# Kernel tuning notes

Hardware: AMD Instinct MI355X
Metric: run time of the kernel (lower is better)

## Reference

```python
import jax, jax.numpy as jnp
import numpy as np

TOP_K = 2  # num_experts_per_tok


def setup_inputs() -> dict:
    key = jax.random.key(0)
    ks = jax.random.split(key, 5)
    B, S, D, M, E = 4, 2048, 2048, 2048, 8
    x = jax.random.normal(ks[0], (B, S, D), dtype=jnp.float32)
    gate_kernel = jax.random.normal(ks[1], (D, E), dtype=jnp.float32) / np.sqrt(D)
    wi_0 = jax.random.normal(ks[2], (E, D, M), dtype=jnp.float32) / np.sqrt(D)
    wi_1 = jax.random.normal(ks[3], (E, D, M), dtype=jnp.float32) / np.sqrt(D)
    wo = jax.random.normal(ks[4], (E, M, D), dtype=jnp.float32) / np.sqrt(M)
    return {"x": x, "gate_kernel": gate_kernel, "wi_0": wi_0, "wi_1": wi_1, "wo": wo}


def reference(x, gate_kernel, wi_0, wi_1, wo):
    E = gate_kernel.shape[-1]
    # Gate logits: (B, S, E)
    gate_logits = jnp.einsum("bsd,de->bse", x, gate_kernel)
    # Top-k routing, then softmax over the selected experts' logits
    top_k_weights, top_k_indices = jax.lax.top_k(gate_logits, TOP_K)
    top_k_weights = jax.nn.softmax(top_k_weights.astype(jnp.float32), axis=-1).astype(x.dtype)
    # Dense combine weights per expert: (B, S, E)
    combine_w = jnp.sum(
        jax.nn.one_hot(top_k_indices, E, dtype=x.dtype) * top_k_weights[..., None], axis=-2
    )
    # Grouped GEMM (dense-masked form, as in MaxText dense_matmul path)
    h0 = jnp.einsum("bsd,edm->bsem", x, wi_0)  # (B, S, E, M)
    h1 = jnp.einsum("bsd,edm->bsem", x, wi_1)
    h = jax.nn.silu(h0) * h1 * combine_w[..., None]
    out = jnp.einsum("bsem,emd->bsd", h, wo)  # (B, S, D)
    return out
```

## Files before the change

kernel.cpp:

```cpp
#include <hip/hip_runtime.h>
#include <hip/hip_bf16.h>
#include <stdint.h>

#define TT   8192
#define DD   2048
#define MM   2048
#define NE   8

typedef float f32x4 __attribute__((ext_vector_type(4)));
typedef short s16x8 __attribute__((ext_vector_type(8)));
typedef unsigned int u32;
typedef unsigned long long u64;

static __device__ __forceinline__ short f2bf(float f) {
  __hip_bfloat16 h = __float2bfloat16(f);
  short s;
  __builtin_memcpy(&s, &h, 2);
  return s;
}

static __device__ __forceinline__ void gload_lds16(const short* g, short* lds) {
  __builtin_amdgcn_global_load_lds(
      (const __attribute__((address_space(1))) u32*)g,
      (__attribute__((address_space(3))) u32*)lds, 16, 0, 0);
}

__global__ __launch_bounds__(256) void tcvt_kernel(
    const float* __restrict__ w0, const float* __restrict__ w1, const float* __restrict__ w2,
    short* __restrict__ o0, short* __restrict__ o1, short* __restrict__ o2) {
  __shared__ short tile[64][65];
  const int bz = blockIdx.z;
  const float* in; short* out;
  if (bz < 8)       { in = w0; out = o0; }
  else if (bz < 16) { in = w1; out = o1; }
  else              { in = w2; out = o2; }
  const int ex = bz & 7;
  const float* src = in + (size_t)ex * DD * MM;
  short* dst = out + (size_t)ex * DD * MM;
  const int r0 = blockIdx.y * 64;
  const int c0 = blockIdx.x * 64;
  const int t = threadIdx.x;
  const int rr = t >> 4, cc = (t & 15) * 4;
  #pragma unroll
  for (int i = 0; i < 4; i++) {
    int row = rr + i * 16;
    f32x4 v = *(const f32x4*)(src + (size_t)(r0 + row) * MM + c0 + cc);
    tile[cc + 0][row] = f2bf(v[0]);
    tile[cc + 1][row] = f2bf(v[1]);
    tile[cc + 2][row] = f2bf(v[2]);
    tile[cc + 3][row] = f2bf(v[3]);
  }
  __syncthreads();
  const int orow = t >> 2, c8 = (t & 3) * 16;
  s16x8 v0, v1;
  #pragma unroll
  for (int i = 0; i < 8; i++) { v0[i] = tile[orow][c8 + i]; v1[i] = tile[orow][c8 + 8 + i]; }
  short* dp = dst + (size_t)(c0 + orow) * DD + r0 + c8;
  *(s16x8*)(dp) = v0;
  *(s16x8*)(dp + 8) = v1;
}

__global__ __launch_bounds__(256) void gate_kernel(const float* __restrict__ x,
    const float* __restrict__ gk, int* __restrict__ counts,
    int* __restrict__ tkidx, float* __restrict__ tkw, short* __restrict__ xbf) {
  int t = blockIdx.x;
  const float* xr = x + (size_t)t * DD;
  const int d0 = threadIdx.x * 8;
  f32x4 a = *(const f32x4*)(xr + d0);
  f32x4 b = *(const f32x4*)(xr + d0 + 4);
  s16x8 v;
  v[0]=f2bf(a[0]); v[1]=f2bf(a[1]); v[2]=f2bf(a[2]); v[3]=f2bf(a[3]);
  v[4]=f2bf(b[0]); v[5]=f2bf(b[1]); v[6]=f2bf(b[2]); v[7]=f2bf(b[3]);
  *(s16x8*)(xbf + (size_t)t * DD + d0) = v;

  float acc[NE];
  #pragma unroll
  for (int e = 0; e < NE; e++) acc[e] = 0.f;
  #pragma unroll
  for (int j = 0; j < 8; j++) {
    float xv = (j < 4) ? a[j] : b[j - 4];
    const float* g = gk + (size_t)(d0 + j) * NE;
    #pragma unroll
    for (int e = 0; e < NE; e++) acc[e] += xv * g[e];
  }
  #pragma unroll
  for (int e = 0; e < NE; e++) {
    #pragma unroll
    for (int off = 32; off >= 1; off >>= 1)
      acc[e] += __shfl_xor(acc[e], off, 64);
  }
  __shared__ float red[4][NE];
  int wid = threadIdx.x >> 6;
  int lane = threadIdx.x & 63;
  if (lane == 0) {
    #pragma unroll
    for (int e = 0; e < NE; e++) red[wid][e] = acc[e];
  }
  __syncthreads();
  if (threadIdx.x == 0) {
    float l[NE];
    #pragma unroll
    for (int e = 0; e < NE; e++) l[e] = red[0][e] + red[1][e] + red[2][e] + red[3][e];
    int i1 = 0; float v1 = l[0];
    #pragma unroll
    for (int e = 1; e < NE; e++) if (l[e] > v1) { v1 = l[e]; i1 = e; }
    int i2 = -1; float v2 = -1e30f;
    #pragma unroll
    for (int e = 0; e < NE; e++) if (e != i1 && l[e] > v2) { v2 = l[e]; i2 = e; }
    float p = __expf(v2 - v1);
    float inv = 1.f / (1.f + p);
    tkidx[t*2]   = i1; tkidx[t*2+1] = i2;
    tkw[t*2]     = inv; tkw[t*2+1]  = p * inv;
    atomicAdd(&counts[i1], 1);
    atomicAdd(&counts[i2], 1);
  }
}

__global__ __launch_bounds__(256) void scatter_kernel(const int* __restrict__ counts,
    int* __restrict__ offsets, const int* __restrict__ tkidx,
    const float* __restrict__ tkw, int* __restrict__ ltok, float* __restrict__ lwt,
    int* __restrict__ slots) {
  const int e = blockIdx.x;
  const int tid = threadIdx.x;
  const int wid = tid >> 6, lane = tid & 63;
  __shared__ int base_s;
  __shared__ int wsum[4];
  if (tid == 0) {
    int s = 0;
    #pragma unroll
    for (int i = 0; i < NE; i++) {
      if (e == 0) offsets[i] = s;
      if (i < e) s += counts[i];
      else if (e == 0) s += counts[i];
    }
    if (e == 0) offsets[NE] = s;
    int bs = 0;
    for (int i = 0; i < e; i++) bs += counts[i];
    base_s = bs;
  }
  __syncthreads();
  int base = base_s;
  for (int it = 0; it < (TT * 2) / 256; it++) {
    int i = it * 256 + tid;
    bool m = (tkidx[i] == e);
    u64 b = __ballot(m);
    if (lane == 0) wsum[wid] = __popcll(b);
    __syncthreads();
    int pre = 0;
    #pragma unroll
    for (int w = 0; w < 4; w++) if (w < wid) pre += wsum[w];
    int tot = wsum[0] + wsum[1] + wsum[2] + wsum[3];
    int rank = __popcll(b & ((lane == 0) ? 0ull : ((1ull << lane) - 1ull)));
    if (m) {
      int dst = base + pre + rank;
      ltok[dst] = i >> 1;
      lwt[dst]  = tkw[i];
      slots[i]  = dst;
    }
    __syncthreads();
    base += tot;
  }
}

__global__ __launch_bounds__(256) void combine_kernel(const float* __restrict__ comb,
    const int* __restrict__ slots, float* __restrict__ out) {
  const int t = blockIdx.x;
  const int s0 = slots[2 * t], s1 = slots[2 * t + 1];
  const f32x4* p0 = (const f32x4*)(comb + (size_t)s0 * DD);
  const f32x4* p1 = (const f32x4*)(comb + (size_t)s1 * DD);
  f32x4* po = (f32x4*)(out + (size_t)t * DD);
  #pragma unroll
  for (int i = 0; i < 2; i++) {
    int idx = threadIdx.x + i * 256;
    po[idx] = p0[idx] + p1[idx];
  }
}

__device__ __forceinline__ void find_seg(const int* __restrict__ offsets, int tile, int bm,
                                         int& e, int& row0, int& rows, int& seg) {
  e = -1; row0 = 0; rows = 0; seg = 0;
  int accT = 0, prev = offsets[0];
  #pragma unroll
  for (int i = 0; i < NE; i++) {
    int nxt = offsets[i+1];
    int cnt = nxt - prev;
    int nt = (cnt + bm - 1) / bm;
    if (e < 0 && tile < accT + nt) { e = i; row0 = (tile - accT) * bm; rows = cnt; seg = prev; }
    accT += nt; prev = nxt;
  }
}

__device__ __forceinline__ void xcd_map(int ypx, int& tile, int& nyi) {
  const int bid = blockIdx.y * gridDim.x + blockIdx.x;
  const int xcd = bid & 7;
  const int i = bid >> 3;
  tile = i / ypx;
  nyi  = xcd * ypx + (i % ypx);
}

#define MAXT1 136

__global__ __launch_bounds__(256, 2) void gemm1_fast(
    const short* __restrict__ xbf,
    const short* __restrict__ w0t, const short* __restrict__ w1t,
    const int* __restrict__ offsets,
    const int* __restrict__ ltok, const float* __restrict__ lwt,
    short* __restrict__ hbuf) {
  __shared__ short As[128 * 64];
  __shared__ short B0s[128 * 64];
  __shared__ short B1s[128 * 64];
  __shared__ float w_s[128];

  int tile, nyi;
  xcd_map(2, tile, nyi);
  const int n0 = nyi * 128;
  int e, row0, rows, seg;
  find_seg(offsets, tile, 128, e, row0, rows, seg);
  if (e < 0) return;

  const int tid = threadIdx.x;
  const int lane = tid & 63, wid = tid >> 6;
  if (tid < 128) {
    int gr = row0 + tid;
    w_s[tid] = (gr < rows) ? lwt[seg + gr] : 0.f;
  }

  const int swz = ((lane & 7) ^ (lane >> 3)) * 8;
  const short* abase[4];
  const short* b0base[4];
  const short* b1base[4];
  #pragma unroll
  for (int c = 0; c < 4; c++) {
    int chunk = wid * 4 + c;
    int r = chunk * 8 + (lane >> 3);
    int gr = row0 + r; if (gr >= rows) gr = rows - 1;
    int tok = ltok[seg + gr];
    abase[c]  = xbf + (size_t)tok * DD + swz;
    int n = n0 + r;
    b0base[c] = w0t + ((size_t)e * MM + n) * DD + swz;
    b1base[c] = w1t + ((size_t)e * MM + n) * DD + swz;
  }

  const int wr = wid >> 1, wc = wid & 1;
  const int lr = lane & 15;
  const int kq = (lane >> 4) * 8;

  f32x4 acc0[4][4], acc1[4][4];
  #pragma unroll
  for (int i = 0; i < 4; i++)
    #pragma unroll
    for (int j = 0; j < 4; j++) { acc0[i][j] = 0.f; acc1[i][j] = 0.f; }

  for (int k0 = 0; k0 < DD; k0 += 64) {
    #pragma unroll
    for (int c = 0; c < 4; c++) {
      int chunk = wid * 4 + c;
      gload_lds16(abase[c]  + k0, As  + chunk * 512);
      gload_lds16(b0base[c] + k0, B0s + chunk * 512);
      gload_lds16(b1base[c] + k0, B1s + chunk * 512);
    }
    __syncthreads();

    #pragma unroll
    for (int ks = 0; ks < 2; ks++) {
      s16x8 a[4], b0[4], b1[4];
      #pragma unroll
      for (int mi = 0; mi < 4; mi++) {
        int row = wr * 64 + mi * 16 + lr;
        int koff = (ks * 32 + kq) ^ ((row & 7) * 8);
        a[mi] = *(const s16x8*)&As[row * 64 + koff];
      }
      #pragma unroll
      for (int ni = 0; ni < 4; ni++) {
        int row = wc * 64 + ni * 16 + lr;
        int koff = (ks * 32 + kq) ^ ((row & 7) * 8);
        b0[ni] = *(const s16x8*)&B0s[row * 64 + koff];
        b1[ni] = *(const s16x8*)&B1s[row * 64 + koff];
      }
      #pragma unroll
      for (int mi = 0; mi < 4; mi++)
        #pragma unroll
        for (int ni = 0; ni < 4; ni++) {
          acc0[mi][ni] = __builtin_amdgcn_mfma_f32_16x16x32_bf16(a[mi], b0[ni], acc0[mi][ni], 0, 0, 0);
          acc1[mi][ni] = __builtin_amdgcn_mfma_f32_16x16x32_bf16(a[mi], b1[ni], acc1[mi][ni], 0, 0, 0);
        }
    }
    __syncthreads();
  }

  const int lq = lane >> 4;
  #pragma unroll
  for (int mi = 0; mi < 4; mi++) {
    #pragma unroll
    for (int jj = 0; jj < 4; jj++) {
      int r = wr * 64 + mi * 16 + lq * 4 + jj;
      int gr = row0 + r;
      if (gr < rows) {
        float wgt = w_s[r];
        size_t hrow = (size_t)(seg + gr) * MM + n0;
        #pragma unroll
        for (int ni = 0; ni < 4; ni++) {
          int c = wc * 64 + ni * 16 + lr;
          float g = acc0[mi][ni][jj];
          float u = acc1[mi][ni][jj];
          float act = g / (1.f + __expf(-g));
          hbuf[hrow + c] = f2bf(act * u * wgt);
        }
      }
    }
  }
}

#define MAXT2 264

__global__ __launch_bounds__(256, 2) void gemm2_fast(
    const short* __restrict__ hbuf,
    const short* __restrict__ wot,
    const int* __restrict__ offsets,
    float* __restrict__ comb) {
  __shared__ short As[64 * 64];
  __shared__ short B0s[128 * 64];
  __shared__ short B1s[128 * 64];

  int tile, nyi;
  xcd_map(1, tile, nyi);
  const int n0 = nyi * 256;
  int e, row0, rows, seg;
  find_seg(offsets, tile, 64, e, row0, rows, seg);
  if (e < 0) return;

  const int tid = threadIdx.x;
  const int lane = tid & 63, wid = tid >> 6;

  const int swz = ((lane & 7) ^ (lane >> 3)) * 8;
  const short* abase[2];
  #pragma unroll
  for (int c = 0; c < 2; c++) {
    int chunk = wid * 2 + c;
    int r = chunk * 8 + (lane >> 3);
    int gr = row0 + r; if (gr >= rows) gr = rows - 1;
    abase[c] = hbuf + (size_t)(seg + gr) * MM + swz;
  }
  const short* b0base[4];
  const short* b1base[4];
  #pragma unroll
  for (int c = 0; c < 4; c++) {
    int chunk = wid * 4 + c;
    int r = chunk * 8 + (lane >> 3);
    b0base[c] = wot + ((size_t)e * DD + n0 + r) * MM + swz;
    b1base[c] = wot + ((size_t)e * DD + n0 + 128 + r) * MM + swz;
  }

  const int wr = wid >> 1, wc = wid & 1;
  const int lr = lane & 15;
  const int kq = (lane >> 4) * 8;

  f32x4 acc0[2][4], acc1[2][4];
  #pragma unroll
  for (int i = 0; i < 2; i++)
    #pragma unroll
    for (int j = 0; j < 4; j++) { acc0[i][j] = 0.f; acc1[i][j] = 0.f; }

  for (int k0 = 0; k0 < MM; k0 += 64) {
    #pragma unroll
    for (int c = 0; c < 2; c++) {
      int chunk = wid * 2 + c;
      gload_lds16(abase[c] + k0, As + chunk * 512);
    }
    #pragma unroll
    for (int c = 0; c < 4; c++) {
      int chunk = wid * 4 + c;
      gload_lds16(b0base[c] + k0, B0s + chunk * 512);
      gload_lds16(b1base[c] + k0, B1s + chunk * 512);
    }
    __syncthreads();

    #pragma unroll
    for (int ks = 0; ks < 2; ks++) {
      s16x8 a[2], b0[4], b1[4];
      #pragma unroll
      for (int mi = 0; mi < 2; mi++) {
        int row = wr * 32 + mi * 16 + lr;
        int koff = (ks * 32 + kq) ^ ((row & 7) * 8);
        a[mi] = *(const s16x8*)&As[row * 64 + koff];
      }
      #pragma unroll
      for (int ni = 0; ni < 4; ni++) {
        int row = wc * 64 + ni * 16 + lr;
        int koff = (ks * 32 + kq) ^ ((row & 7) * 8);
        b0[ni] = *(const s16x8*)&B0s[row * 64 + koff];
        b1[ni] = *(const s16x8*)&B1s[row * 64 + koff];
      }
      #pragma unroll
      for (int mi = 0; mi < 2; mi++)
        #pragma unroll
        for (int ni = 0; ni < 4; ni++) {
          acc0[mi][ni] = __builtin_amdgcn_mfma_f32_16x16x32_bf16(a[mi], b0[ni], acc0[mi][ni], 0, 0, 0);
          acc1[mi][ni] = __builtin_amdgcn_mfma_f32_16x16x32_bf16(a[mi], b1[ni], acc1[mi][ni], 0, 0, 0);
        }
    }
    __syncthreads();
  }

  const int lq = lane >> 4;
  #pragma unroll
  for (int mi = 0; mi < 2; mi++) {
    #pragma unroll
    for (int jj = 0; jj < 4; jj++) {
      int r = wr * 32 + mi * 16 + lq * 4 + jj;
      int gr = row0 + r;
      if (gr < rows) {
        size_t orow = (size_t)(seg + gr) * DD + n0;
        #pragma unroll
        for (int ni = 0; ni < 4; ni++) {
          int c = wc * 64 + ni * 16 + lr;
          comb[orow + c] = acc0[mi][ni][jj];
          comb[orow + 128 + c] = acc1[mi][ni][jj];
        }
      }
    }
  }
}

extern "C" void kernel_launch(void* const* d_in, const int* in_sizes, int n_in,
                              void* d_out, int out_size, void* d_ws, size_t ws_size,
                              hipStream_t stream) {
  const float* x   = (const float*)d_in[0];
  const float* gk  = (const float*)d_in[1];
  const float* wi0 = (const float*)d_in[2];
  const float* wi1 = (const float*)d_in[3];
  const float* wo  = (const float*)d_in[4];
  float* out = (float*)d_out;

  char* w = (char*)d_ws;
  int*   counts  = (int*)(w);
  int*   offsets = (int*)(w + 256);
  int*   tkidx   = (int*)(w + 1024);
  float* tkw     = (float*)(w + 1024 + 65536);
  int*   ltok    = (int*)(w + 1024 + 2*65536);
  float* lwt     = (float*)(w + 1024 + 3*65536);
  int*   slots   = (int*)(w + 1024 + 4*65536);
  short* xbf  = (short*)(w + 524288);
  short* hbuf = xbf + (size_t)TT * DD;
  short* w0t  = hbuf + (size_t)2 * TT * MM;
  short* w1t  = w0t + (size_t)NE * DD * MM;
  short* wot  = w1t + (size_t)NE * DD * MM;
  float* comb = (float*)w0t;

  hipMemsetAsync(counts, 0, 64, stream);

  gate_kernel<<<TT, 256, 0, stream>>>(x, gk, counts, tkidx, tkw, xbf);
  scatter_kernel<<<NE, 256, 0, stream>>>(counts, offsets, tkidx, tkw, ltok, lwt, slots);
  tcvt_kernel<<<dim3(MM/64, DD/64, 24), 256, 0, stream>>>(wi0, wi1, wo, w0t, w1t, wot);

  gemm1_fast<<<dim3(MAXT1, MM/128), 256, 0, stream>>>(xbf, w0t, w1t, offsets, ltok, lwt, hbuf);
  gemm2_fast<<<dim3(MAXT2, DD/256), 256, 0, stream>>>(hbuf, wot, offsets, comb);
  combine_kernel<<<TT, 256, 0, stream>>>(comb, slots, out);
}
```

Measured before the change: 904.8 us.

## Rewrite gemm2 with 256x256 tiles, double-buffered LDS pipeline, and bf16 combine buffer

The down-projection GEMM now uses 512-thread blocks with 256x256 output tiles. Its LDS is double-buffered, and global-to-LDS prefetch is interleaved with MFMA phases using explicit vmcnt waits, barriers and setprio. This raises data reuse per tile and hides load latency. The intermediate per-slot outputs are also stored as bf16 instead of fp32, which halves combine traffic at some precision cost. The larger tiles waste more work on partially filled expert segments, and the hand-written waitcnt scheduling risks races.

Measured after the change: 890.7 us. No clear change (-1.6%).

```diff
diff --git a/kernel.cpp b/kernel.cpp
--- a/kernel.cpp
+++ b/kernel.cpp
@@ -18,12 +18,23 @@
   __builtin_memcpy(&s, &h, 2);
   return s;
 }
+static __device__ __forceinline__ float bf2f(short s) {
+  u32 u = ((u32)(unsigned short)s) << 16;
+  float f;
+  __builtin_memcpy(&f, &u, 4);
+  return f;
+}
 
 static __device__ __forceinline__ void gload_lds16(const short* g, short* lds) {
   __builtin_amdgcn_global_load_lds(
       (const __attribute__((address_space(1))) u32*)g,
       (__attribute__((address_space(3))) u32*)lds, 16, 0, 0);
 }
+
+#define VM2()  asm volatile("s_waitcnt vmcnt(2)" ::: "memory")
+#define VM0()  asm volatile("s_waitcnt vmcnt(0)" ::: "memory")
+#define LG0()  asm volatile("s_waitcnt lgkmcnt(0)" ::: "memory")
+#define BAR()  __builtin_amdgcn_s_barrier()
 
 __global__ __launch_bounds__(256) void tcvt_kernel(
     const float* __restrict__ w0, const float* __restrict__ w1, const float* __restrict__ w2,
@@ -162,18 +173,22 @@
   }
 }
 
-__global__ __launch_bounds__(256) void combine_kernel(const float* __restrict__ comb,
+__global__ __launch_bounds__(256) void combine_kernel(const short* __restrict__ comb,
     const int* __restrict__ slots, float* __restrict__ out) {
   const int t = blockIdx.x;
   const int s0 = slots[2 * t], s1 = slots[2 * t + 1];
-  const f32x4* p0 = (const f32x4*)(comb + (size_t)s0 * DD);
-  const f32x4* p1 = (const f32x4*)(comb + (size_t)s1 * DD);
-  f32x4* po = (f32x4*)(out + (size_t)t * DD);
-  #pragma unroll
-  for (int i = 0; i < 2; i++) {
-    int idx = threadIdx.x + i * 256;
-    po[idx] = p0[idx] + p1[idx];
-  }
+  const int idx = threadIdx.x;
+  s16x8 a = *(const s16x8*)(comb + (size_t)s0 * DD + idx * 8);
+  s16x8 b = *(const s16x8*)(comb + (size_t)s1 * DD + idx * 8);
+  f32x4 o0, o1;
+  #pragma unroll
+  for (int j = 0; j < 4; j++) {
+    o0[j] = bf2f(a[j]) + bf2f(b[j]);
+    o1[j] = bf2f(a[4 + j]) + bf2f(b[4 + j]);
+  }
+  float* po = out + (size_t)t * DD + idx * 8;
+  *(f32x4*)(po) = o0;
+  *(f32x4*)(po + 4) = o1;
 }
 
 __device__ __forceinline__ void find_seg(const int* __restrict__ offsets, int tile, int bm,
@@ -311,111 +326,231 @@
   }
 }
 
-#define MAXT2 264
-
-__global__ __launch_bounds__(256, 2) void gemm2_fast(
+#define MAXT2 72
+
+__global__ __launch_bounds__(512, 2) void gemm2_fast(
     const short* __restrict__ hbuf,
     const short* __restrict__ wot,
     const int* __restrict__ offsets,
-    float* __restrict__ comb) {
-  __shared__ short As[64 * 64];
-  __shared__ short B0s[128 * 64];
-  __shared__ short B1s[128 * 64];
+    short* __restrict__ comb) {
+  __shared__ short As[2][256 * 64];
+  __shared__ short Bs[2][256 * 64];
 
   int tile, nyi;
   xcd_map(1, tile, nyi);
   const int n0 = nyi * 256;
   int e, row0, rows, seg;
-  find_seg(offsets, tile, 64, e, row0, rows, seg);
+  find_seg(offsets, tile, 256, e, row0, rows, seg);
   if (e < 0) return;
 
   const int tid = threadIdx.x;
   const int lane = tid & 63, wid = tid >> 6;
-
-  const int swz = ((lane & 7) ^ (lane >> 3)) * 8;
-  const short* abase[2];
-  #pragma unroll
-  for (int c = 0; c < 2; c++) {
-    int chunk = wid * 2 + c;
-    int r = chunk * 8 + (lane >> 3);
-    int gr = row0 + r; if (gr >= rows) gr = rows - 1;
-    abase[c] = hbuf + (size_t)(seg + gr) * MM + swz;
-  }
-  const short* b0base[4];
-  const short* b1base[4];
-  #pragma unroll
-  for (int c = 0; c < 4; c++) {
-    int chunk = wid * 4 + c;
-    int r = chunk * 8 + (lane >> 3);
-    b0base[c] = wot + ((size_t)e * DD + n0 + r) * MM + swz;
-    b1base[c] = wot + ((size_t)e * DD + n0 + 128 + r) * MM + swz;
-  }
-
-  const int wr = wid >> 1, wc = wid & 1;
+  const int srow = tid >> 3;
+  const int swz = ((tid & 7) ^ (srow & 7)) * 8;
+
+  const short* aP[2][2];
+  const short* bP[2][2];
+  #pragma unroll
+  for (int h = 0; h < 2; h++)
+    #pragma unroll
+    for (int rd = 0; rd < 2; rd++) {
+      int gr = row0 + h * 128 + rd * 64 + srow;
+      if (gr >= rows) gr = rows - 1;
+      aP[h][rd] = hbuf + (size_t)(seg + gr) * MM + swz;
+      int n = n0 + h * 128 + rd * 64 + srow;
+      bP[h][rd] = wot + ((size_t)e * DD + n) * MM + swz;
+    }
+  const short* aP00 = aP[0][0]; const short* aP01 = aP[0][1];
+  const short* aP10 = aP[1][0]; const short* aP11 = aP[1][1];
+  const short* bP00 = bP[0][0]; const short* bP01 = bP[0][1];
+  const short* bP10 = bP[1][0]; const short* bP11 = bP[1][1];
+
+  const int wr = wid >> 2, wn = wid & 3;
   const int lr = lane & 15;
   const int kq = (lane >> 4) * 8;
-
-  f32x4 acc0[2][4], acc1[2][4];
-  #pragma unroll
-  for (int i = 0; i < 2; i++)
-    #pragma unroll
-    for (int j = 0; j < 4; j++) { acc0[i][j] = 0.f; acc1[i][j] = 0.f; }
-
-  for (int k0 = 0; k0 < MM; k0 += 64) {
-    #pragma unroll
-    for (int c = 0; c < 2; c++) {
-      int chunk = wid * 2 + c;
-      gload_lds16(abase[c] + k0, As + chunk * 512);
-    }
-    #pragma unroll
-    for (int c = 0; c < 4; c++) {
-      int chunk = wid * 4 + c;
-      gload_lds16(b0base[c] + k0, B0s + chunk * 512);
-      gload_lds16(b1base[c] + k0, B1s + chunk * 512);
-    }
-    __syncthreads();
-
-    #pragma unroll
-    for (int ks = 0; ks < 2; ks++) {
-      s16x8 a[2], b0[4], b1[4];
-      #pragma unroll
-      for (int mi = 0; mi < 2; mi++) {
-        int row = wr * 32 + mi * 16 + lr;
-        int koff = (ks * 32 + kq) ^ ((row & 7) * 8);
-        a[mi] = *(const s16x8*)&As[row * 64 + koff];
-      }
-      #pragma unroll
-      for (int ni = 0; ni < 4; ni++) {
-        int row = wc * 64 + ni * 16 + lr;
-        int koff = (ks * 32 + kq) ^ ((row & 7) * 8);
-        b0[ni] = *(const s16x8*)&B0s[row * 64 + koff];
-        b1[ni] = *(const s16x8*)&B1s[row * 64 + koff];
-      }
-      #pragma unroll
-      for (int mi = 0; mi < 2; mi++)
-        #pragma unroll
-        for (int ni = 0; ni < 4; ni++) {
-          acc0[mi][ni] = __builtin_amdgcn_mfma_f32_16x16x32_bf16(a[mi], b0[ni], acc0[mi][ni], 0, 0, 0);
-          acc1[mi][ni] = __builtin_amdgcn_mfma_f32_16x16x32_bf16(a[mi], b1[ni], acc1[mi][ni], 0, 0, 0);
-        }
-    }
-    __syncthreads();
-  }
-
   const int lq = lane >> 4;
-  #pragma unroll
-  for (int mi = 0; mi < 2; mi++) {
+
+  f32x4 acc[8][4];
+  #pragma unroll
+  for (int i = 0; i < 8; i++)
+    #pragma unroll
+    for (int j = 0; j < 4; j++) acc[i][j] = 0.f;
+
+  int brow_[4], bkey_[4];
+  #pragma unroll
+  for (int ni = 0; ni < 4; ni++) {
+    brow_[ni] = wn * 64 + ni * 16 + lr;
+    bkey_[ni] = (brow_[ni] & 7) * 8;
+  }
+  int arowL_[4], akeyL_[4], arowH_[4], akeyH_[4];
+  #pragma unroll
+  for (int mi = 0; mi < 4; mi++) {
+    arowL_[mi] = wr * 128 + mi * 16 + lr;        akeyL_[mi] = (arowL_[mi] & 7) * 8;
+    arowH_[mi] = wr * 128 + (mi + 4) * 16 + lr;  akeyH_[mi] = (arowH_[mi] & 7) * 8;
+  }
+
+  const int wofs = wid * 512;
+  auto stA0 = [&](int buf, int kof) {
+    short* d = &As[buf][0];
+    gload_lds16(aP00 + kof, d + wofs);
+    gload_lds16(aP01 + kof, d + 4096 + wofs);
+  };
+  auto stA1 = [&](int buf, int kof) {
+    short* d = &As[buf][128 * 64];
+    gload_lds16(aP10 + kof, d + wofs);
+    gload_lds16(aP11 + kof, d + 4096 + wofs);
+  };
+  auto stB0 = [&](int buf, int kof) {
+    short* d = &Bs[buf][0];
+    gload_lds16(bP00 + kof, d + wofs);
+    gload_lds16(bP01 + kof, d + 4096 + wofs);
+  };
+  auto stB1 = [&](int buf, int kof) {
+    short* d = &Bs[buf][128 * 64];
+    gload_lds16(bP10 + kof, d + wofs);
+    gload_lds16(bP11 + kof, d + 4096 + wofs);
+  };
+
+  stA0(0, 0); stB0(0, 0); stB1(0, 0); stA1(0, 0);
+  stA0(1, 64);
+  VM2();
+  BAR();
+
+  const int NIT = (MM / 64) / 2;
+  s16x8 av[4], bv[4], bw[4];
+
+  for (int it = 0; it < NIT; ++it) {
+    const bool pf = (it + 1 < NIT);
+    const int kb  = (2 * it + 1) * 64;
+    const int kna = (2 * it + 2) * 64;
+    const int knb = (2 * it + 3) * 64;
+
+    #pragma unroll
+    for (int mi = 0; mi < 4; mi++) av[mi] = *(const s16x8*)&As[0][arowL_[mi] * 64 + (kq ^ akeyL_[mi])];
+    #pragma unroll
+    for (int ni = 0; ni < 4; ni++) bv[ni] = *(const s16x8*)&Bs[0][brow_[ni] * 64 + (kq ^ bkey_[ni])];
+    stB0(1, kb);
+    BAR(); LG0();
+    __builtin_amdgcn_s_setprio(1);
+    #pragma unroll
+    for (int mi = 0; mi < 4; mi++)
+      #pragma unroll
+      for (int ni = 0; ni < 4; ni++)
+        acc[mi][ni] = __builtin_amdgcn_mfma_f32_16x16x32_bf16(av[mi], bv[ni], acc[mi][ni], 0, 0, 0);
+    __builtin_amdgcn_s_setprio(0);
+    BAR();
+
+    #pragma unroll
+    for (int mi = 0; mi < 4; mi++) av[mi] = *(const s16x8*)&As[0][arowH_[mi] * 64 + (kq ^ akeyH_[mi])];
+    stB1(1, kb);
+    BAR(); LG0();
+    __builtin_amdgcn_s_setprio(1);
+    #pragma unroll
+    for (int mi = 0; mi < 4; mi++)
+      #pragma unroll
+      for (int ni = 0; ni < 4; ni++)
+        acc[mi + 4][ni] = __builtin_amdgcn_mfma_f32_16x16x32_bf16(av[mi], bv[ni], acc[mi + 4][ni], 0, 0, 0);
+    __builtin_amdgcn_s_setprio(0);
+    BAR();
+
+    #pragma unroll
+    for (int mi = 0; mi < 4; mi++) av[mi] = *(const s16x8*)&As[0][arowL_[mi] * 64 + ((32 + kq) ^ akeyL_[mi])];
+    #pragma unroll
+    for (int ni = 0; ni < 4; ni++) bw[ni] = *(const s16x8*)&Bs[0][brow_[ni] * 64 + ((32 + kq) ^ bkey_[ni])];
+    stA1(1, kb);
+    BAR(); LG0();
+    __builtin_amdgcn_s_setprio(1);
+    #pragma unroll
+    for (int mi = 0; mi < 4; mi++)
+      #pragma unroll
+      for (int ni = 0; ni < 4; ni++)
+        acc[mi][ni] = __builtin_amdgcn_mfma_f32_16x16x32_bf16(av[mi], bw[ni], acc[mi][ni], 0, 0, 0);
+    __builtin_amdgcn_s_setprio(0);
+    BAR();
+
+    #pragma unroll
+    for (int mi = 0; mi < 4; mi++) av[mi] = *(const s16x8*)&As[0][arowH_[mi] * 64 + ((32 + kq) ^ akeyH_[mi])];
+    if (pf) stA0(0, kna);
+    BAR(); LG0();
+    __builtin_amdgcn_s_setprio(1);
+    #pragma unroll
+    for (int mi = 0; mi < 4; mi++)
+      #pragma unroll
+      for (int ni = 0; ni < 4; ni++)
+        acc[mi + 4][ni] = __builtin_amdgcn_mfma_f32_16x16x32_bf16(av[mi], bw[ni], acc[mi + 4][ni], 0, 0, 0);
+    __builtin_amdgcn_s_setprio(0);
+    if (pf) { VM2(); } else { VM0(); }
+    BAR();
+
+    #pragma unroll
+    for (int mi = 0; mi < 4; mi++) av[mi] = *(const s16x8*)&As[1][arowL_[mi] * 64 + (kq ^ akeyL_[mi])];
+    #pragma unroll
+    for (int ni = 0; ni < 4; ni++) bv[ni] = *(const s16x8*)&Bs[1][brow_[ni] * 64 + (kq ^ bkey_[ni])];
+    if (pf) stB0(0, kna);
+    BAR(); LG0();
+    __builtin_amdgcn_s_setprio(1);
+    #pragma unroll
+    for (int mi = 0; mi < 4; mi++)
+      #pragma unroll
+      for (int ni = 0; ni < 4; ni++)
+        acc[mi][ni] = __builtin_amdgcn_mfma_f32_16x16x32_bf16(av[mi], bv[ni], acc[mi][ni], 0, 0, 0);
+    __builtin_amdgcn_s_setprio(0);
+    BAR();
+
+    #pragma unroll
+    for (int mi = 0; mi < 4; mi++) av[mi] = *(const s16x8*)&As[1][arowH_[mi] * 64 + (kq ^ akeyH_[mi])];
+    if (pf) stB1(0, kna);
+    BAR(); LG0();
+    __builtin_amdgcn_s_setprio(1);
+    #pragma unroll
+    for (int mi = 0; mi < 4; mi++)
+      #pragma unroll
+      for (int ni = 0; ni < 4; ni++)
+        acc[mi + 4][ni] = __builtin_amdgcn_mfma_f32_16x16x32_bf16(av[mi], bv[ni], acc[mi + 4][ni], 0, 0, 0);
+    __builtin_amdgcn_s_setprio(0);
+    BAR();
+
+    #pragma unroll
+    for (int mi = 0; mi < 4; mi++) av[mi] = *(const s16x8*)&As[1][arowL_[mi] * 64 + ((32 + kq) ^ akeyL_[mi])];
+    #pragma unroll
+    for (int ni = 0; ni < 4; ni++) bw[ni] = *(const s16x8*)&Bs[1][brow_[ni] * 64 + ((32 + kq) ^ bkey_[ni])];
+    if (pf) stA1(0, kna);
+    BAR(); LG0();
+    __builtin_amdgcn_s_setprio(1);
+    #pragma unroll
+    for (int mi = 0; mi < 4; mi++)
+      #pragma unroll
+      for (int ni = 0; ni < 4; ni++)
+        acc[mi][ni] = __builtin_amdgcn_mfma_f32_16x16x32_bf16(av[mi], bw[ni], acc[mi][ni], 0, 0, 0);
+    __builtin_amdgcn_s_setprio(0);
+    BAR();
+
+    #pragma unroll
+    for (int mi = 0; mi < 4; mi++) av[mi] = *(const s16x8*)&As[1][arowH_[mi] * 64 + ((32 + kq) ^ akeyH_[mi])];
+    if (pf) stA0(1, knb);
+    BAR(); LG0();
+    __builtin_amdgcn_s_setprio(1);
+    #pragma unroll
+    for (int mi = 0; mi < 4; mi++)
+      #pragma unroll
+      for (int ni = 0; ni < 4; ni++)
+        acc[mi + 4][ni] = __builtin_amdgcn_mfma_f32_16x16x32_bf16(av[mi], bw[ni], acc[mi + 4][ni], 0, 0, 0);
+    __builtin_amdgcn_s_setprio(0);
+    if (pf) { VM2(); BAR(); }
+  }
+
+  #pragma unroll
+  for (int mi = 0; mi < 8; mi++) {
     #pragma unroll
     for (int jj = 0; jj < 4; jj++) {
-      int r = wr * 32 + mi * 16 + lq * 4 + jj;
+      int r = wr * 128 + mi * 16 + lq * 4 + jj;
       int gr = row0 + r;
       if (gr < rows) {
         size_t orow = (size_t)(seg + gr) * DD + n0;
         #pragma unroll
         for (int ni = 0; ni < 4; ni++) {
-          int c = wc * 64 + ni * 16 + lr;
-          comb[orow + c] = acc0[mi][ni][jj];
-          comb[orow + 128 + c] = acc1[mi][ni][jj];
+          int c = wn * 64 + ni * 16 + lr;
+          comb[orow + c] = f2bf(acc[mi][ni][jj]);
         }
       }
     }
@@ -445,7 +580,7 @@
   short* w0t  = hbuf + (size_t)2 * TT * MM;
   short* w1t  = w0t + (size_t)NE * DD * MM;
   short* wot  = w1t + (size_t)NE * DD * MM;
-  float* comb = (float*)w0t;
+  short* comb = w0t;
 
   hipMemsetAsync(counts, 0, 64, stream);
 
@@ -454,6 +589,6 @@
   tcvt_kernel<<<dim3(MM/64, DD/64, 24), 256, 0, stream>>>(wi0, wi1, wo, w0t, w1t, wot);
 
   gemm1_fast<<<dim3(MAXT1, MM/128), 256, 0, stream>>>(xbf, w0t, w1t, offsets, ltok, lwt, hbuf);
-  gemm2_fast<<<dim3(MAXT2, DD/256), 256, 0, stream>>>(hbuf, wot, offsets, comb);
+  gemm2_fast<<<dim3(MAXT2, DD/256), 512, 0, stream>>>(hbuf, wot, offsets, comb);
   combine_kernel<<<TT, 256, 0, stream>>>(comb, slots, out);
 }
```

## Fuse weight conversion into gate and gemm1, enlarge gemm2 tile, bf16 combine buffer

Applied to the files above, without the earlier changes.

Folds the wi0/wi1 bf16 transpose-convert blocks into the gate kernel launch and the wo conversion into the gemm1 launch as extra blocks, so conversion overlaps other work and one launch goes away. gemm2 moves from 64-row to 128-row M tiles, doubling accumulators per wave. The per-slot combine buffer is stored in bf16 instead of fp32, halving its write and read traffic. This costs extra output rounding, higher register pressure in gemm2, and wo-conversion blocks now contend with gemm1 compute.

Result: faster. 839.2 us, median of 2 (-7.3%).

```diff
diff --git a/kernel.cpp b/kernel.cpp
--- a/kernel.cpp
+++ b/kernel.cpp
@@ -18,6 +18,12 @@
   __builtin_memcpy(&s, &h, 2);
   return s;
 }
+static __device__ __forceinline__ float bf2f(short s) {
+  u32 u = ((u32)(unsigned short)s) << 16;
+  float f;
+  __builtin_memcpy(&f, &u, 4);
+  return f;
+}
 
 static __device__ __forceinline__ void gload_lds16(const short* g, short* lds) {
   __builtin_amdgcn_global_load_lds(
@@ -25,45 +31,52 @@
       (__attribute__((address_space(3))) u32*)lds, 16, 0, 0);
 }
 
-__global__ __launch_bounds__(256) void tcvt_kernel(
-    const float* __restrict__ w0, const float* __restrict__ w1, const float* __restrict__ w2,
-    short* __restrict__ o0, short* __restrict__ o1, short* __restrict__ o2) {
+#define GCVT01  (16 * 32 * 32)
+
+__global__ __launch_bounds__(256) void gate_fused(
+    const float* __restrict__ x, const float* __restrict__ gk,
+    int* __restrict__ counts, int* __restrict__ tkidx, float* __restrict__ tkw,
+    short* __restrict__ xbf,
+    const float* __restrict__ wi0, const float* __restrict__ wi1,
+    short* __restrict__ o0, short* __restrict__ o1) {
   __shared__ short tile[64][65];
-  const int bz = blockIdx.z;
-  const float* in; short* out;
-  if (bz < 8)       { in = w0; out = o0; }
-  else if (bz < 16) { in = w1; out = o1; }
-  else              { in = w2; out = o2; }
-  const int ex = bz & 7;
-  const float* src = in + (size_t)ex * DD * MM;
-  short* dst = out + (size_t)ex * DD * MM;
-  const int r0 = blockIdx.y * 64;
-  const int c0 = blockIdx.x * 64;
-  const int t = threadIdx.x;
-  const int rr = t >> 4, cc = (t & 15) * 4;
-  #pragma unroll
-  for (int i = 0; i < 4; i++) {
-    int row = rr + i * 16;
-    f32x4 v = *(const f32x4*)(src + (size_t)(r0 + row) * MM + c0 + cc);
-    tile[cc + 0][row] = f2bf(v[0]);
-    tile[cc + 1][row] = f2bf(v[1]);
-    tile[cc + 2][row] = f2bf(v[2]);
-    tile[cc + 3][row] = f2bf(v[3]);
-  }
-  __syncthreads();
-  const int orow = t >> 2, c8 = (t & 3) * 16;
-  s16x8 v0, v1;
-  #pragma unroll
-  for (int i = 0; i < 8; i++) { v0[i] = tile[orow][c8 + i]; v1[i] = tile[orow][c8 + 8 + i]; }
-  short* dp = dst + (size_t)(c0 + orow) * DD + r0 + c8;
-  *(s16x8*)(dp) = v0;
-  *(s16x8*)(dp + 8) = v1;
-}
-
-__global__ __launch_bounds__(256) void gate_kernel(const float* __restrict__ x,
-    const float* __restrict__ gk, int* __restrict__ counts,
-    int* __restrict__ tkidx, float* __restrict__ tkw, short* __restrict__ xbf) {
-  int t = blockIdx.x;
+  __shared__ float red[4][NE];
+
+  const int bid = blockIdx.x;
+  if (bid >= TT) {
+    const int idx = bid - TT;
+    const int wz = idx >> 10;
+    const float* in  = (wz < 8) ? wi0 : wi1;
+    short* out       = (wz < 8) ? o0 : o1;
+    const int ex = wz & 7;
+    const int rem = idx & 1023;
+    const int r0 = (rem >> 5) * 64;
+    const int c0 = (rem & 31) * 64;
+    const float* src = in + (size_t)ex * DD * MM;
+    short* dst = out + (size_t)ex * DD * MM;
+    const int t = threadIdx.x;
+    const int rr = t >> 4, cc = (t & 15) * 4;
+    #pragma unroll
+    for (int i = 0; i < 4; i++) {
+      int row = rr + i * 16;
+      f32x4 v = *(const f32x4*)(src + (size_t)(r0 + row) * MM + c0 + cc);
+      tile[cc + 0][row] = f2bf(v[0]);
+      tile[cc + 1][row] = f2bf(v[1]);
+      tile[cc + 2][row] = f2bf(v[2]);
+      tile[cc + 3][row] = f2bf(v[3]);
+    }
+    __syncthreads();
+    const int orow = t >> 2, c8 = (t & 3) * 16;
+    s16x8 v0, v1;
+    #pragma unroll
+    for (int i = 0; i < 8; i++) { v0[i] = tile[orow][c8 + i]; v1[i] = tile[orow][c8 + 8 + i]; }
+    short* dp = dst + (size_t)(c0 + orow) * DD + r0 + c8;
+    *(s16x8*)(dp) = v0;
+    *(s16x8*)(dp + 8) = v1;
+    return;
+  }
+
+  const int t = bid;
   const float* xr = x + (size_t)t * DD;
   const int d0 = threadIdx.x * 8;
   f32x4 a = *(const f32x4*)(xr + d0);
@@ -89,7 +102,6 @@
     for (int off = 32; off >= 1; off >>= 1)
       acc[e] += __shfl_xor(acc[e], off, 64);
   }
-  __shared__ float red[4][NE];
   int wid = threadIdx.x >> 6;
   int lane = threadIdx.x & 63;
   if (lane == 0) {
@@ -162,18 +174,22 @@
   }
 }
 
-__global__ __launch_bounds__(256) void combine_kernel(const float* __restrict__ comb,
+__global__ __launch_bounds__(256) void combine_kernel(const short* __restrict__ comb,
     const int* __restrict__ slots, float* __restrict__ out) {
   const int t = blockIdx.x;
   const int s0 = slots[2 * t], s1 = slots[2 * t + 1];
-  const f32x4* p0 = (const f32x4*)(comb + (size_t)s0 * DD);
-  const f32x4* p1 = (const f32x4*)(comb + (size_t)s1 * DD);
-  f32x4* po = (f32x4*)(out + (size_t)t * DD);
-  #pragma unroll
-  for (int i = 0; i < 2; i++) {
-    int idx = threadIdx.x + i * 256;
-    po[idx] = p0[idx] + p1[idx];
-  }
+  const int idx = threadIdx.x;
+  s16x8 a = *(const s16x8*)(comb + (size_t)s0 * DD + idx * 8);
+  s16x8 b = *(const s16x8*)(comb + (size_t)s1 * DD + idx * 8);
+  f32x4 o0, o1;
+  #pragma unroll
+  for (int j = 0; j < 4; j++) {
+    o0[j] = bf2f(a[j]) + bf2f(b[j]);
+    o1[j] = bf2f(a[4 + j]) + bf2f(b[4 + j]);
+  }
+  float* po = out + (size_t)t * DD + idx * 8;
+  *(f32x4*)(po) = o0;
+  *(f32x4*)(po + 4) = o1;
 }
 
 __device__ __forceinline__ void find_seg(const int* __restrict__ offsets, int tile, int bm,
@@ -198,21 +214,58 @@
   nyi  = xcd * ypx + (i % ypx);
 }
 
-#define MAXT1 136
-
-__global__ __launch_bounds__(256, 2) void gemm1_fast(
+#define G1TILES 136
+#define G1GRID  (G1TILES * 16)
+#define GOGRID  (8 * 32 * 32)
+
+__global__ __launch_bounds__(256, 2) void gemm1_fused(
     const short* __restrict__ xbf,
     const short* __restrict__ w0t, const short* __restrict__ w1t,
     const int* __restrict__ offsets,
     const int* __restrict__ ltok, const float* __restrict__ lwt,
-    short* __restrict__ hbuf) {
+    short* __restrict__ hbuf,
+    const float* __restrict__ wo, short* __restrict__ wot) {
   __shared__ short As[128 * 64];
   __shared__ short B0s[128 * 64];
   __shared__ short B1s[128 * 64];
   __shared__ float w_s[128];
 
-  int tile, nyi;
-  xcd_map(2, tile, nyi);
+  const int bid = blockIdx.x;
+  if (bid >= G1GRID) {
+    short (*tile)[65] = (short(*)[65])As;
+    const int idx = bid - G1GRID;
+    const int ex = idx >> 10;
+    const int rem = idx & 1023;
+    const int r0 = (rem >> 5) * 64;
+    const int c0 = (rem & 31) * 64;
+    const float* src = wo + (size_t)ex * DD * MM;
+    short* dst = wot + (size_t)ex * DD * MM;
+    const int t = threadIdx.x;
+    const int rr = t >> 4, cc = (t & 15) * 4;
+    #pragma unroll
+    for (int i = 0; i < 4; i++) {
+      int row = rr + i * 16;
+      f32x4 v = *(const f32x4*)(src + (size_t)(r0 + row) * MM + c0 + cc);
+      tile[cc + 0][row] = f2bf(v[0]);
+      tile[cc + 1][row] = f2bf(v[1]);
+      tile[cc + 2][row] = f2bf(v[2]);
+      tile[cc + 3][row] = f2bf(v[3]);
+    }
+    __syncthreads();
+    const int orow = t >> 2, c8 = (t & 3) * 16;
+    s16x8 v0, v1;
+    #pragma unroll
+    for (int i = 0; i < 8; i++) { v0[i] = tile[orow][c8 + i]; v1[i] = tile[orow][c8 + 8 + i]; }
+    short* dp = dst + (size_t)(c0 + orow) * DD + r0 + c8;
+    *(s16x8*)(dp) = v0;
+    *(s16x8*)(dp + 8) = v1;
+    return;
+  }
+
+  const int xcd = bid & 7;
+  const int bi = bid >> 3;
+  const int tile = bi >> 1;
+  const int nyi = xcd * 2 + (bi & 1);
   const int n0 = nyi * 128;
   int e, row0, rows, seg;
   find_seg(offsets, tile, 128, e, row0, rows, seg);
@@ -311,14 +364,12 @@
   }
 }
 
-#define MAXT2 264
-
 __global__ __launch_bounds__(256, 2) void gemm2_fast(
     const short* __restrict__ hbuf,
     const short* __restrict__ wot,
     const int* __restrict__ offsets,
-    float* __restrict__ comb) {
-  __shared__ short As[64 * 64];
+    short* __restrict__ comb) {
+  __shared__ short As[128 * 64];
   __shared__ short B0s[128 * 64];
   __shared__ short B1s[128 * 64];
 
@@ -326,27 +377,22 @@
   xcd_map(1, tile, nyi);
   const int n0 = nyi * 256;
   int e, row0, rows, seg;
-  find_seg(offsets, tile, 64, e, row0, rows, seg);
+  find_seg(offsets, tile, 128, e, row0, rows, seg);
   if (e < 0) return;
 
   const int tid = threadIdx.x;
   const int lane = tid & 63, wid = tid >> 6;
 
   const int swz = ((lane & 7) ^ (lane >> 3)) * 8;
-  const short* abase[2];
-  #pragma unroll
-  for (int c = 0; c < 2; c++) {
-    int chunk = wid * 2 + c;
+  const short* abase[4];
+  const short* b0base[4];
+  const short* b1base[4];
+  #pragma unroll
+  for (int c = 0; c < 4; c++) {
+    int chunk = wid * 4 + c;
     int r = chunk * 8 + (lane >> 3);
     int gr = row0 + r; if (gr >= rows) gr = rows - 1;
     abase[c] = hbuf + (size_t)(seg + gr) * MM + swz;
-  }
-  const short* b0base[4];
-  const short* b1base[4];
-  #pragma unroll
-  for (int c = 0; c < 4; c++) {
-    int chunk = wid * 4 + c;
-    int r = chunk * 8 + (lane >> 3);
     b0base[c] = wot + ((size_t)e * DD + n0 + r) * MM + swz;
     b1base[c] = wot + ((size_t)e * DD + n0 + 128 + r) * MM + swz;
   }
@@ -355,21 +401,17 @@
   const int lr = lane & 15;
   const int kq = (lane >> 4) * 8;
 
-  f32x4 acc0[2][4], acc1[2][4];
-  #pragma unroll
-  for (int i = 0; i < 2; i++)
+  f32x4 acc0[4][4], acc1[4][4];
+  #pragma unroll
+  for (int i = 0; i < 4; i++)
     #pragma unroll
     for (int j = 0; j < 4; j++) { acc0[i][j] = 0.f; acc1[i][j] = 0.f; }
 
   for (int k0 = 0; k0 < MM; k0 += 64) {
-    #pragma unroll
-    for (int c = 0; c < 2; c++) {
-      int chunk = wid * 2 + c;
-      gload_lds16(abase[c] + k0, As + chunk * 512);
-    }
     #pragma unroll
     for (int c = 0; c < 4; c++) {
       int chunk = wid * 4 + c;
+      gload_lds16(abase[c]  + k0, As  + chunk * 512);
       gload_lds16(b0base[c] + k0, B0s + chunk * 512);
       gload_lds16(b1base[c] + k0, B1s + chunk * 512);
     }
@@ -377,10 +419,10 @@
 
     #pragma unroll
     for (int ks = 0; ks < 2; ks++) {
-      s16x8 a[2], b0[4], b1[4];
+      s16x8 a[4], b0[4], b1[4];
       #pragma unroll
-      for (int mi = 0; mi < 2; mi++) {
-        int row = wr * 32 + mi * 16 + lr;
+      for (int mi = 0; mi < 4; mi++) {
+        int row = wr * 64 + mi * 16 + lr;
         int koff = (ks * 32 + kq) ^ ((row & 7) * 8);
         a[mi] = *(const s16x8*)&As[row * 64 + koff];
       }
@@ -392,7 +434,7 @@
         b1[ni] = *(const s16x8*)&B1s[row * 64 + koff];
       }
       #pragma unroll
-      for (int mi = 0; mi < 2; mi++)
+      for (int mi = 0; mi < 4; mi++)
         #pragma unroll
         for (int ni = 0; ni < 4; ni++) {
           acc0[mi][ni] = __builtin_amdgcn_mfma_f32_16x16x32_bf16(a[mi], b0[ni], acc0[mi][ni], 0, 0, 0);
@@ -404,18 +446,18 @@
 
   const int lq = lane >> 4;
   #pragma unroll
-  for (int mi = 0; mi < 2; mi++) {
+  for (int mi = 0; mi < 4; mi++) {
     #pragma unroll
     for (int jj = 0; jj < 4; jj++) {
-      int r = wr * 32 + mi * 16 + lq * 4 + jj;
+      int r = wr * 64 + mi * 16 + lq * 4 + jj;
       int gr = row0 + r;
       if (gr < rows) {
         size_t orow = (size_t)(seg + gr) * DD + n0;
         #pragma unroll
         for (int ni = 0; ni < 4; ni++) {
           int c = wc * 64 + ni * 16 + lr;
-          comb[orow + c] = acc0[mi][ni][jj];
-          comb[orow + 128 + c] = acc1[mi][ni][jj];
+          comb[orow + c] = f2bf(acc0[mi][ni][jj]);
+          comb[orow + 128 + c] = f2bf(acc1[mi][ni][jj]);
         }
       }
     }
@@ -445,15 +487,16 @@
   short* w0t  = hbuf + (size_t)2 * TT * MM;
   short* w1t  = w0t + (size_t)NE * DD * MM;
   short* wot  = w1t + (size_t)NE * DD * MM;
-  float* comb = (float*)w0t;
+  short* comb = w0t;
 
   hipMemsetAsync(counts, 0, 64, stream);
 
-  gate_kernel<<<TT, 256, 0, stream>>>(x, gk, counts, tkidx, tkw, xbf);
+  gate_fused<<<TT + GCVT01, 256, 0, stream>>>(x, gk, counts, tkidx, tkw, xbf,
+                                              wi0, wi1, w0t, w1t);
   scatter_kernel<<<NE, 256, 0, stream>>>(counts, offsets, tkidx, tkw, ltok, lwt, slots);
-  tcvt_kernel<<<dim3(MM/64, DD/64, 24), 256, 0, stream>>>(wi0, wi1, wo, w0t, w1t, wot);
-
-  gemm1_fast<<<dim3(MAXT1, MM/128), 256, 0, stream>>>(xbf, w0t, w1t, offsets, ltok, lwt, hbuf);
-  gemm2_fast<<<dim3(MAXT2, DD/256), 256, 0, stream>>>(hbuf, wot, offsets, comb);
+
+  gemm1_fused<<<G1GRID + GOGRID, 256, 0, stream>>>(xbf, w0t, w1t, offsets, ltok, lwt,
+                                                   hbuf, wo, wot);
+  gemm2_fast<<<dim3(G1TILES, DD/256), 256, 0, stream>>>(hbuf, wot, offsets, comb);
   combine_kernel<<<TT, 256, 0, stream>>>(comb, slots, out);
 }
```
